# Kernel tuning notes

Measured on AMD Instinct MI355X. Metric: run time of the kernel, lower is better.

## Reference

```python
import jax, jax.numpy as jnp
import numpy as np

N = 200_000      # active voxels
C_IN = 128
C_OUT = 128
GRID = 128
K = 27           # 3x3x3 submanifold kernel offsets
EPS = 1e-4       # scn BatchNormalization default eps
LEAK = 0.333     # scn LeakyReLU default leakiness


def _build_neighbor_idx(rng):
    # unique active voxel coords via unique linear keys in GRID^3
    keys = rng.choice(GRID ** 3, size=N, replace=False).astype(np.int64)
    z = keys % GRID
    y = (keys // GRID) % GRID
    x = keys // (GRID * GRID)
    coords = np.stack([x, y, z], axis=1)  # [N,3]
    order = np.argsort(keys)
    sorted_keys = keys[order]
    offs = np.array([(dx, dy, dz) for dx in (-1, 0, 1)
                     for dy in (-1, 0, 1) for dz in (-1, 0, 1)], dtype=np.int64)
    nb = np.full((N, K), -1, dtype=np.int32)
    for k in range(K):
        q = coords + offs[k]  # [N,3]
        inb = np.all((q >= 0) & (q < GRID), axis=1)
        qk = (q[:, 0] * GRID + q[:, 1]) * GRID + q[:, 2]
        pos = np.searchsorted(sorted_keys, qk)
        pos = np.clip(pos, 0, N - 1)
        hit = inb & (sorted_keys[pos] == qk)
        nb[:, k] = np.where(hit, order[pos].astype(np.int32), -1)
    return nb


def setup_inputs() -> dict:
    key = jax.random.key(0)
    k1, k2 = jax.random.split(key)
    rng = np.random.default_rng(0)
    neighbor_idx = jnp.asarray(_build_neighbor_idx(rng))       # [N,27] int32, -1 = inactive
    features = jax.random.normal(k1, (N, C_IN), dtype=jnp.float32)
    # per-offset conv weights, scn-style init scale
    W = jax.random.normal(k2, (K, C_IN, C_OUT), dtype=jnp.float32) * (1.0 / np.sqrt(K * C_IN))
    b = jnp.zeros((C_OUT,), dtype=jnp.float32)
    gamma = jnp.ones((C_OUT,), dtype=jnp.float32)
    beta = jnp.zeros((C_OUT,), dtype=jnp.float32)
    return {"features": features, "W": W, "b": b, "gamma": gamma,
            "beta": beta, "neighbor_idx": neighbor_idx}


def reference(features, W, b, gamma, beta, neighbor_idx):
    # Submanifold 3D conv: output only at active sites; gather active neighbors.
    valid = (neighbor_idx >= 0)                      # [N,27] bool
    idx = jnp.where(valid, neighbor_idx, 0)          # safe gather index
    out = jnp.broadcast_to(b, (features.shape[0], C_OUT))
    for k in range(K):  # fixed structural loop over 27 kernel offsets
        xk = features[idx[:, k]] * valid[:, k:k + 1].astype(features.dtype)  # [N,C_IN]
        out = out + xk @ W[k]                                                # [N,C_OUT]
    # BatchNormalization over all active sites (training-mode batch stats)
    mean = jnp.mean(out, axis=0)
    var = jnp.var(out, axis=0)
    out = (out - mean) * jax.lax.rsqrt(var + EPS) * gamma + beta
    # LeakyReLU (scn default leakiness 0.333)
    return jnp.where(out > 0, out, LEAK * out)
```

## Files before the change

### kernel.cpp

```cpp
#include <hip/hip_runtime.h>
#include <hip/hip_bf16.h>

#define N_VOX 200000
#define CI 128
#define CO 128
#define KK 27
#define BM 128
#define NBLK 1563
#define NSTEP 54
#define LEAK 0.333f
#define BN_EPS 1e-4f

typedef unsigned short u16;
typedef unsigned int u32;
typedef __attribute__((ext_vector_type(8))) short short8;
typedef __attribute__((ext_vector_type(4))) float f32x4;

typedef const __attribute__((address_space(1))) u32* gptr_t;
typedef __attribute__((address_space(3))) u32* lptr_t;

__device__ __forceinline__ u16 f2bf(float f) {
  union { float f; u32 u; } x; x.f = f;
  return (u16)((x.u + 0x7FFFu + ((x.u >> 16) & 1u)) >> 16);
}
__device__ __forceinline__ u16 cvt_bf(float f) {
  union { __hip_bfloat16 h; u16 u; } c;
  c.h = __float2bfloat16(f);
  return c.u;
}

__global__ __launch_bounds__(256) void fcast_kernel(const float* __restrict__ f,
                                                    u16* __restrict__ fb) {
  size_t i = ((size_t)blockIdx.x * 256 + threadIdx.x) * 8;
  float4 a = *(const float4*)(f + i);
  float4 b = *(const float4*)(f + i + 4);
  u16 t[8];
  t[0] = cvt_bf(a.x); t[1] = cvt_bf(a.y); t[2] = cvt_bf(a.z); t[3] = cvt_bf(a.w);
  t[4] = cvt_bf(b.x); t[5] = cvt_bf(b.y); t[6] = cvt_bf(b.z); t[7] = cvt_bf(b.w);
  *(uint4*)(fb + i) = *(const uint4*)t;
}

__global__ __launch_bounds__(256) void wcast_kernel(const float* __restrict__ W,
                                                    u16* __restrict__ Wt) {
  __shared__ float tile[32][33];
  int k = blockIdx.z;
  int ci0 = blockIdx.y * 32, co0 = blockIdx.x * 32;
  const float* Wk = W + (size_t)k * CI * CO;
  u16* Wtk = Wt + (size_t)k * CI * CO;
  int tx = threadIdx.x, ty = threadIdx.y;
#pragma unroll
  for (int j = 0; j < 4; ++j)
    tile[ty + j * 8][tx] = Wk[(ci0 + ty + j * 8) * CO + co0 + tx];
  __syncthreads();
#pragma unroll
  for (int j = 0; j < 4; ++j) {
    int co = co0 + ty + j * 8;
    int ci = ci0 + tx;
    Wtk[co * CI + (ci ^ ((co & 7) << 3))] = f2bf(tile[tx][ty + j * 8]);
  }
}

__global__ __launch_bounds__(256, 2) void conv_kernel(
    const u16* __restrict__ featb, const u16* __restrict__ Wt,
    const int* __restrict__ nb, const u16* __restrict__ zp,
    float* __restrict__ out, float* __restrict__ partial) {
  __shared__ __align__(16) char smem[79360];
  u16* const Ab0 = (u16*)smem;
  u16* const Ab1 = (u16*)(smem + 16384);
  u16* const Bb0 = (u16*)(smem + 32768);
  u16* const Bb1 = (u16*)(smem + 49152);
  int* const nbs = (int*)(smem + 65536);
  float* const sq = (float*)smem;

  const int tid = threadIdx.x;
  const int bid = blockIdx.x;
  const int row0 = bid * BM;

  for (int i = tid; i < BM * KK; i += 256) {
    int gi = row0 * KK + i;
    nbs[i] = (gi < N_VOX * KK) ? nb[gi] : -1;
  }
  __syncthreads();

  const int lane = tid & 63;
  const int wv = tid >> 6;
  const int wr = wv >> 1, wc = wv & 1;
  const int lr = lane & 15, lg = lane >> 4;

  f32x4 acc[4][4];
#pragma unroll
  for (int m = 0; m < 4; ++m)
#pragma unroll
    for (int n = 0; n < 4; ++n) acc[m][n] = (f32x4){0.f, 0.f, 0.f, 0.f};

  auto issueA = [&](int s, u16* Adst) {
    int k = s >> 1;
    int halfU = (s & 1) * 64;
    int r = tid >> 3;
    int cl = tid & 7;
#pragma unroll
    for (int j = 0; j < 4; ++j) {
      int row = j * 32 + r;
      int src = nbs[row * KK + k];
      const u16* g = (src >= 0) ? (featb + (size_t)src * CI + halfU) : zp;
      g += ((cl ^ (row & 7)) << 3);
      __builtin_amdgcn_global_load_lds((gptr_t)g, (lptr_t)(Adst + (j * 32 + wv * 8) * 64),
                                       16, 0, 0);
    }
  };

  auto issueB = [&](int s, u16* Bdst) {
    int k = s >> 1;
    int halfU = (s & 1) * 64;
    const u16* base = Wt + (size_t)k * CI * CO + halfU;
#pragma unroll
    for (int j = 0; j < 4; ++j) {
      int cb = (j * 4 + wv) * 64;
      int c = cb + lane;
      int co = c >> 3, sub = c & 7;
      __builtin_amdgcn_global_load_lds((gptr_t)(base + co * CI + sub * 8),
                                       (lptr_t)(Bdst + cb * 8), 16, 0, 0);
    }
  };

  auto compute = [&](const u16* A, const u16* B) {
    __builtin_amdgcn_s_setprio(1);
#pragma unroll
    for (int ks = 0; ks < 2; ++ks) {
      short8 a[4], b[4];
#pragma unroll
      for (int m = 0; m < 4; ++m) {
        int r = wr * 64 + m * 16 + lr;
        a[m] = *(const short8*)((const char*)(A + r * 64) +
                                ((ks * 64 + lg * 16) ^ ((r & 7) << 4)));
      }
#pragma unroll
      for (int n = 0; n < 4; ++n) {
        int cn = wc * 64 + n * 16 + lr;
        b[n] = *(const short8*)((const char*)(B + cn * 64) +
                                ((ks * 64 + lg * 16) ^ ((cn & 7) << 4)));
      }
#pragma unroll
      for (int m = 0; m < 4; ++m)
#pragma unroll
        for (int n = 0; n < 4; ++n)
          acc[m][n] = __builtin_amdgcn_mfma_f32_16x16x32_bf16(a[m], b[n], acc[m][n], 0, 0, 0);
    }
    __builtin_amdgcn_s_setprio(0);
  };

  issueA(0, Ab0);
  issueB(0, Bb0);
  for (int s = 0; s < NSTEP; ++s) {
    __syncthreads();
    int pb = s & 1;
    if (s + 1 < NSTEP) {
      issueA(s + 1, pb ? Ab0 : Ab1);
      issueB(s + 1, pb ? Bb0 : Bb1);
    }
    compute(pb ? Ab1 : Ab0, pb ? Bb1 : Bb0);
  }

  float sv[4], qv[4];
#pragma unroll
  for (int n = 0; n < 4; ++n) {
    float s = 0.f, q = 0.f;
    int col = wc * 64 + n * 16 + lr;
#pragma unroll
    for (int m = 0; m < 4; ++m) {
      int rb = row0 + wr * 64 + m * 16 + lg * 4;
#pragma unroll
      for (int e = 0; e < 4; ++e) {
        float x = acc[m][n][e];
        if (rb + e < N_VOX) out[(size_t)(rb + e) * CO + col] = x;
        s += x; q += x * x;
      }
    }
    s += __shfl_xor(s, 16, 64); s += __shfl_xor(s, 32, 64);
    q += __shfl_xor(q, 16, 64); q += __shfl_xor(q, 32, 64);
    sv[n] = s; qv[n] = q;
  }
  __syncthreads();
  if (lg == 0) {
#pragma unroll
    for (int n = 0; n < 4; ++n) {
      int col = wc * 64 + n * 16 + lr;
      sq[wr * 256 + col] = sv[n];
      sq[wr * 256 + 128 + col] = qv[n];
    }
  }
  __syncthreads();
  partial[(size_t)bid * 256 + tid] = sq[tid] + sq[256 + tid];
}

__global__ __launch_bounds__(256, 2) void conv_fb_kernel(
    const float* __restrict__ feat, const u16* __restrict__ Wt,
    const int* __restrict__ nb, float* __restrict__ out,
    float* __restrict__ partial) {
  __shared__ __align__(16) char smem[79360];
  u16* const Ab0 = (u16*)smem;
  u16* const Ab1 = (u16*)(smem + 16384);
  u16* const Bb0 = (u16*)(smem + 32768);
  u16* const Bb1 = (u16*)(smem + 49152);
  int* const nbs = (int*)(smem + 65536);
  float* const sq = (float*)smem;

  const int tid = threadIdx.x;
  const int bid = blockIdx.x;
  const int row0 = bid * BM;

  for (int i = tid; i < BM * KK; i += 256) {
    int gi = row0 * KK + i;
    nbs[i] = (gi < N_VOX * KK) ? nb[gi] : -1;
  }
  __syncthreads();

  const int lane = tid & 63;
  const int wv = tid >> 6;
  const int wr = wv >> 1, wc = wv & 1;
  const int lr = lane & 15, lg = lane >> 4;
  const int arow = tid >> 1;
  const int acol = (tid & 1) * 32;

  f32x4 acc[4][4];
#pragma unroll
  for (int m = 0; m < 4; ++m)
#pragma unroll
    for (int n = 0; n < 4; ++n) acc[m][n] = (f32x4){0.f, 0.f, 0.f, 0.f};

  float4 af[8];
  auto issueA = [&](int s) {
    int k = s >> 1, half = (s & 1) * 64;
    int src = nbs[arow * KK + k];
    if (src >= 0) {
      const float4* p = (const float4*)(feat + (size_t)src * CI + half + acol);
#pragma unroll
      for (int j = 0; j < 8; ++j) af[j] = p[j];
    } else {
#pragma unroll
      for (int j = 0; j < 8; ++j) af[j] = (float4){0.f, 0.f, 0.f, 0.f};
    }
  };
  auto issueB = [&](int s, u16* Bdst) {
    int k = s >> 1, half = (s & 1) * 64;
    const u16* base = Wt + (size_t)k * CO * CI + half;
#pragma unroll
    for (int j = 0; j < 4; ++j) {
      int cb = (j * 4 + wv) * 64;
      int c = cb + lane;
      int co = c >> 3, sub = c & 7;
      __builtin_amdgcn_global_load_lds((gptr_t)(base + co * CI + sub * 8),
                                       (lptr_t)(Bdst + cb * 8), 16, 0, 0);
    }
  };
  auto writeA = [&](u16* Adst) {
    int v = arow & 7;
#pragma unroll
    for (int q = 0; q < 4; ++q) {
      u16 t8[8];
#pragma unroll
      for (int i = 0; i < 2; ++i) {
        float4 f = af[q * 2 + i];
        t8[i * 4 + 0] = cvt_bf(f.x); t8[i * 4 + 1] = cvt_bf(f.y);
        t8[i * 4 + 2] = cvt_bf(f.z); t8[i * 4 + 3] = cvt_bf(f.w);
      }
      int c_o = (tid & 1) * 4 + q;
      *(uint4*)&Adst[arow * 64 + ((c_o ^ v) << 3)] = *(const uint4*)t8;
    }
  };
  auto compute = [&](const u16* A, const u16* B) {
#pragma unroll
    for (int ks = 0; ks < 2; ++ks) {
      short8 a[4], b[4];
#pragma unroll
      for (int m = 0; m < 4; ++m) {
        int r = wr * 64 + m * 16 + lr;
        a[m] = *(const short8*)((const char*)(A + r * 64) +
                                ((ks * 64 + lg * 16) ^ ((r & 7) << 4)));
      }
#pragma unroll
      for (int n = 0; n < 4; ++n) {
        int cn = wc * 64 + n * 16 + lr;
        b[n] = *(const short8*)((const char*)(B + cn * 64) +
                                ((ks * 64 + lg * 16) ^ ((cn & 7) << 4)));
      }
#pragma unroll
      for (int m = 0; m < 4; ++m)
#pragma unroll
        for (int n = 0; n < 4; ++n)
          acc[m][n] = __builtin_amdgcn_mfma_f32_16x16x32_bf16(a[m], b[n], acc[m][n], 0, 0, 0);
    }
  };

  issueA(0);
  issueB(0, Bb0);
  for (int s = 0; s < NSTEP - 1; ++s) {
    int pb = s & 1;
    u16* Ac = pb ? Ab1 : Ab0;
    u16* Bc = pb ? Bb1 : Bb0;
    u16* Bn = pb ? Bb0 : Bb1;
    writeA(Ac);
    __syncthreads();
    issueA(s + 1);
    issueB(s + 1, Bn);
    compute(Ac, Bc);
  }
  writeA(Ab1);
  __syncthreads();
  compute(Ab1, Bb1);

  float sv[4], qv[4];
#pragma unroll
  for (int n = 0; n < 4; ++n) {
    float s = 0.f, q = 0.f;
    int col = wc * 64 + n * 16 + lr;
#pragma unroll
    for (int m = 0; m < 4; ++m) {
      int rb = row0 + wr * 64 + m * 16 + lg * 4;
#pragma unroll
      for (int e = 0; e < 4; ++e) {
        float x = acc[m][n][e];
        if (rb + e < N_VOX) out[(size_t)(rb + e) * CO + col] = x;
        s += x; q += x * x;
      }
    }
    s += __shfl_xor(s, 16, 64); s += __shfl_xor(s, 32, 64);
    q += __shfl_xor(q, 16, 64); q += __shfl_xor(q, 32, 64);
    sv[n] = s; qv[n] = q;
  }
  __syncthreads();
  if (lg == 0) {
#pragma unroll
    for (int n = 0; n < 4; ++n) {
      int col = wc * 64 + n * 16 + lr;
      sq[wr * 256 + col] = sv[n];
      sq[wr * 256 + 128 + col] = qv[n];
    }
  }
  __syncthreads();
  partial[(size_t)bid * 256 + tid] = sq[tid] + sq[256 + tid];
}

__global__ __launch_bounds__(256) void reduce1_kernel(const float* __restrict__ partial,
                                                      float* __restrict__ partial2) {
  int t = threadIdx.x, b = blockIdx.x;
  float acc = 0.f;
  int jend = (b + 1) * 16; if (jend > NBLK) jend = NBLK;
  for (int j = b * 16; j < jend; ++j) acc += partial[(size_t)j * 256 + t];
  partial2[(size_t)b * 256 + t] = acc;
}

__global__ __launch_bounds__(256) void reduce2_kernel(const float* __restrict__ partial2,
                                                      const float* __restrict__ gamma,
                                                      const float* __restrict__ beta,
                                                      float* __restrict__ stats) {
  __shared__ float sums[256];
  int t = threadIdx.x;
  float acc = 0.f;
  for (int j = 0; j < 98; ++j) acc += partial2[(size_t)j * 256 + t];
  sums[t] = acc;
  __syncthreads();
  if (t < 128) {
    float mean = sums[t] / (float)N_VOX;
    float var = sums[128 + t] / (float)N_VOX - mean * mean;
    float scale = gamma[t] * rsqrtf(var + BN_EPS);
    stats[t] = scale;
    stats[128 + t] = beta[t] - mean * scale;
  }
}

__global__ __launch_bounds__(256) void bnact_kernel(float* __restrict__ out,
                                                    const float* __restrict__ stats) {
  __shared__ float s_scale[128], s_shift[128];
  int t = threadIdx.x;
  if (t < 128) { s_scale[t] = stats[t]; s_shift[t] = stats[128 + t]; }
  __syncthreads();
  size_t i = (size_t)blockIdx.x * 256 + t;
  float4* o4 = (float4*)out;
  float4 v = o4[i];
  int c0 = ((int)(i & 31)) << 2;
  float x;
  x = v.x * s_scale[c0 + 0] + s_shift[c0 + 0]; v.x = x > 0.f ? x : LEAK * x;
  x = v.y * s_scale[c0 + 1] + s_shift[c0 + 1]; v.y = x > 0.f ? x : LEAK * x;
  x = v.z * s_scale[c0 + 2] + s_shift[c0 + 2]; v.z = x > 0.f ? x : LEAK * x;
  x = v.w * s_scale[c0 + 3] + s_shift[c0 + 3]; v.w = x > 0.f ? x : LEAK * x;
  o4[i] = v;
}

extern "C" void kernel_launch(void* const* d_in, const int* in_sizes, int n_in,
                              void* d_out, int out_size, void* d_ws, size_t ws_size,
                              hipStream_t stream) {
  const float* feat  = (const float*)d_in[0];
  const float* W     = (const float*)d_in[1];
  const float* gamma = (const float*)d_in[3];
  const float* beta  = (const float*)d_in[4];
  const int*   nb    = (const int*)d_in[5];
  float* out = (float*)d_out;

  char* ws = (char*)d_ws;
  u16*   Wt       = (u16*)ws;
  float* partial  = (float*)(ws + 884736);
  float* partial2 = (float*)(ws + 2485248);
  float* stats    = (float*)(ws + 2585600);
  u16*   zp       = (u16*)(ws + 2586624);
  u16*   featb    = (u16*)(ws + 2586880);
  const size_t need_fast = 2586880u + 51200000u;

  hipLaunchKernelGGL(wcast_kernel, dim3(4, 4, 27), dim3(32, 8), 0, stream, W, Wt);
  if (ws_size >= need_fast) {
    hipMemsetAsync(zp, 0, 256, stream);
    hipLaunchKernelGGL(fcast_kernel, dim3(12500), dim3(256), 0, stream, feat, featb);
    hipLaunchKernelGGL(conv_kernel, dim3(NBLK), dim3(256), 0, stream,
                       featb, Wt, nb, zp, out, partial);
  } else {
    hipLaunchKernelGGL(conv_fb_kernel, dim3(NBLK), dim3(256), 0, stream,
                       feat, Wt, nb, out, partial);
  }
  hipLaunchKernelGGL(reduce1_kernel, dim3(98), dim3(256), 0, stream, partial, partial2);
  hipLaunchKernelGGL(reduce2_kernel, dim3(1), dim3(256), 0, stream, partial2, gamma, beta, stats);
  hipLaunchKernelGGL(bnact_kernel, dim3(25000), dim3(256), 0, stream, out, stats);
}
```

Before: 288.9 us.

## Pre-swizzle weights into MFMA fragment layout and deepen the A-gather pipeline

Weights are now pre-cast into a layout matching the MFMA B-operand fragments. Each wave loads its B fragments straight from global memory into registers, so B no longer goes through LDS. The A gather buffer goes from double to four-deep, staged with global_load_lds and a manual vmcnt wait plus a raw barrier, so three steps of gathers are in flight while MFMAs run. This removes LDS traffic and ds_reads for B and hides gather latency better, at the cost of more VGPRs for two B register sets and redundant B loads per wave from L2.

Result: slower. 303.7 us, median of 2 (+5.1%).

```diff
diff --git a/kernel.cpp b/kernel.cpp
--- a/kernel.cpp
+++ b/kernel.cpp
@@ -40,35 +40,26 @@
   *(uint4*)(fb + i) = *(const uint4*)t;
 }
 
-__global__ __launch_bounds__(256) void wcast_kernel(const float* __restrict__ W,
-                                                    u16* __restrict__ Wt) {
-  __shared__ float tile[32][33];
-  int k = blockIdx.z;
-  int ci0 = blockIdx.y * 32, co0 = blockIdx.x * 32;
+__global__ __launch_bounds__(256) void wcast2_kernel(const float* __restrict__ W,
+                                                     u16* __restrict__ Wt2) {
+  int gid = blockIdx.x * 256 + threadIdx.x;
+  int lane = gid & 63, chunk = gid >> 6;
+  int n8 = chunk & 7, ks = (chunk >> 3) & 1, half = (chunk >> 4) & 1, k = chunk >> 5;
+  int lr = lane & 15, lg = lane >> 4;
+  int co = n8 * 16 + lr;
+  int ci0 = half * 64 + ks * 32 + lg * 8;
   const float* Wk = W + (size_t)k * CI * CO;
-  u16* Wtk = Wt + (size_t)k * CI * CO;
-  int tx = threadIdx.x, ty = threadIdx.y;
-#pragma unroll
-  for (int j = 0; j < 4; ++j)
-    tile[ty + j * 8][tx] = Wk[(ci0 + ty + j * 8) * CO + co0 + tx];
-  __syncthreads();
-#pragma unroll
-  for (int j = 0; j < 4; ++j) {
-    int co = co0 + ty + j * 8;
-    int ci = ci0 + tx;
-    Wtk[co * CI + (ci ^ ((co & 7) << 3))] = f2bf(tile[tx][ty + j * 8]);
-  }
+  u16 t[8];
+#pragma unroll
+  for (int e = 0; e < 8; ++e) t[e] = f2bf(Wk[(ci0 + e) * CO + co]);
+  *(uint4*)(Wt2 + (size_t)gid * 8) = *(const uint4*)t;
 }
 
 __global__ __launch_bounds__(256, 2) void conv_kernel(
-    const u16* __restrict__ featb, const u16* __restrict__ Wt,
+    const u16* __restrict__ featb, const u16* __restrict__ Wt2,
     const int* __restrict__ nb, const u16* __restrict__ zp,
     float* __restrict__ out, float* __restrict__ partial) {
   __shared__ __align__(16) char smem[79360];
-  u16* const Ab0 = (u16*)smem;
-  u16* const Ab1 = (u16*)(smem + 16384);
-  u16* const Bb0 = (u16*)(smem + 32768);
-  u16* const Bb1 = (u16*)(smem + 49152);
   int* const nbs = (int*)(smem + 65536);
   float* const sq = (float*)smem;
 
@@ -93,11 +84,14 @@
 #pragma unroll
     for (int n = 0; n < 4; ++n) acc[m][n] = (f32x4){0.f, 0.f, 0.f, 0.f};
 
-  auto issueA = [&](int s, u16* Adst) {
+  short8 b0[8], b1[8];
+
+  auto issueA = [&](int s, int slot) {
+    if (s >= NSTEP) s = NSTEP - 1;
     int k = s >> 1;
     int halfU = (s & 1) * 64;
-    int r = tid >> 3;
-    int cl = tid & 7;
+    u16* Adst = (u16*)(smem + slot * 16384);
+    int r = tid >> 3, cl = tid & 7;
 #pragma unroll
     for (int j = 0; j < 4; ++j) {
       int row = j * 32 + r;
@@ -109,56 +103,55 @@
     }
   };
 
-  auto issueB = [&](int s, u16* Bdst) {
-    int k = s >> 1;
-    int halfU = (s & 1) * 64;
-    const u16* base = Wt + (size_t)k * CI * CO + halfU;
-#pragma unroll
-    for (int j = 0; j < 4; ++j) {
-      int cb = (j * 4 + wv) * 64;
-      int c = cb + lane;
-      int co = c >> 3, sub = c & 7;
-      __builtin_amdgcn_global_load_lds((gptr_t)(base + co * CI + sub * 8),
-                                       (lptr_t)(Bdst + cb * 8), 16, 0, 0);
-    }
-  };
-
-  auto compute = [&](const u16* A, const u16* B) {
+  auto loadB = [&](int s, short8* bn) {
+    if (s >= NSTEP) s = NSTEP - 1;
+    int k = s >> 1, half = s & 1;
+    const u16* base = Wt2 + (((k * 2 + half) * 16 + wc * 4) * 512) + lane * 8;
+#pragma unroll
+    for (int n = 0; n < 4; ++n)
+#pragma unroll
+      for (int ks = 0; ks < 2; ++ks)
+        bn[n * 2 + ks] = *(const short8*)(base + (ks * 8 + n) * 512);
+  };
+
+  auto compute = [&](int slot, const short8* bc) {
+    const char* A = smem + slot * 16384;
     __builtin_amdgcn_s_setprio(1);
 #pragma unroll
     for (int ks = 0; ks < 2; ++ks) {
-      short8 a[4], b[4];
+      short8 a[4];
 #pragma unroll
       for (int m = 0; m < 4; ++m) {
         int r = wr * 64 + m * 16 + lr;
-        a[m] = *(const short8*)((const char*)(A + r * 64) +
-                                ((ks * 64 + lg * 16) ^ ((r & 7) << 4)));
+        a[m] = *(const short8*)(A + r * 128 + ((ks * 64 + lg * 16) ^ ((r & 7) << 4)));
       }
 #pragma unroll
-      for (int n = 0; n < 4; ++n) {
-        int cn = wc * 64 + n * 16 + lr;
-        b[n] = *(const short8*)((const char*)(B + cn * 64) +
-                                ((ks * 64 + lg * 16) ^ ((cn & 7) << 4)));
-      }
-#pragma unroll
       for (int m = 0; m < 4; ++m)
 #pragma unroll
         for (int n = 0; n < 4; ++n)
-          acc[m][n] = __builtin_amdgcn_mfma_f32_16x16x32_bf16(a[m], b[n], acc[m][n], 0, 0, 0);
+          acc[m][n] = __builtin_amdgcn_mfma_f32_16x16x32_bf16(a[m], bc[n * 2 + ks],
+                                                              acc[m][n], 0, 0, 0);
     }
     __builtin_amdgcn_s_setprio(0);
   };
 
-  issueA(0, Ab0);
-  issueB(0, Bb0);
-  for (int s = 0; s < NSTEP; ++s) {
-    __syncthreads();
-    int pb = s & 1;
-    if (s + 1 < NSTEP) {
-      issueA(s + 1, pb ? Ab0 : Ab1);
-      issueB(s + 1, pb ? Bb0 : Bb1);
-    }
-    compute(pb ? Ab1 : Ab0, pb ? Bb1 : Bb0);
+  auto step_body = [&](int s, const short8* bc, short8* bn) {
+    asm volatile("s_waitcnt vmcnt(16)" ::: "memory");
+    __builtin_amdgcn_sched_barrier(0);
+    __builtin_amdgcn_s_barrier();
+    __builtin_amdgcn_sched_barrier(0);
+    loadB(s + 1, bn);
+    issueA(s + 3, (s + 3) & 3);
+    compute(s & 3, bc);
+  };
+
+  issueA(0, 0);
+  issueA(1, 1);
+  loadB(0, b0);
+  issueA(2, 2);
+  for (int s = 0; s < NSTEP; s += 2) {
+    step_body(s, b0, b1);
+    step_body(s + 1, b1, b0);
   }
 
   float sv[4], qv[4];
@@ -194,15 +187,12 @@
 }
 
 __global__ __launch_bounds__(256, 2) void conv_fb_kernel(
-    const float* __restrict__ feat, const u16* __restrict__ Wt,
+    const float* __restrict__ feat, const u16* __restrict__ Wt2,
     const int* __restrict__ nb, float* __restrict__ out,
     float* __restrict__ partial) {
-  __shared__ __align__(16) char smem[79360];
-  u16* const Ab0 = (u16*)smem;
-  u16* const Ab1 = (u16*)(smem + 16384);
-  u16* const Bb0 = (u16*)(smem + 32768);
-  u16* const Bb1 = (u16*)(smem + 49152);
-  int* const nbs = (int*)(smem + 65536);
+  __shared__ __align__(16) char smem[46592];
+  u16* const Ab = (u16*)smem;
+  int* const nbs = (int*)(smem + 32768);
   float* const sq = (float*)smem;
 
   const int tid = threadIdx.x;
@@ -229,7 +219,9 @@
     for (int n = 0; n < 4; ++n) acc[m][n] = (f32x4){0.f, 0.f, 0.f, 0.f};
 
   float4 af[8];
-  auto issueA = [&](int s) {
+  short8 b0[8], b1[8];
+
+  auto issueAf = [&](int s) {
     int k = s >> 1, half = (s & 1) * 64;
     int src = nbs[arow * KK + k];
     if (src >= 0) {
@@ -241,17 +233,14 @@
       for (int j = 0; j < 8; ++j) af[j] = (float4){0.f, 0.f, 0.f, 0.f};
     }
   };
-  auto issueB = [&](int s, u16* Bdst) {
-    int k = s >> 1, half = (s & 1) * 64;
-    const u16* base = Wt + (size_t)k * CO * CI + half;
-#pragma unroll
-    for (int j = 0; j < 4; ++j) {
-      int cb = (j * 4 + wv) * 64;
-      int c = cb + lane;
-      int co = c >> 3, sub = c & 7;
-      __builtin_amdgcn_global_load_lds((gptr_t)(base + co * CI + sub * 8),
-                                       (lptr_t)(Bdst + cb * 8), 16, 0, 0);
-    }
+  auto loadB = [&](int s, short8* bn) {
+    int k = s >> 1, half = s & 1;
+    const u16* base = Wt2 + (((k * 2 + half) * 16 + wc * 4) * 512) + lane * 8;
+#pragma unroll
+    for (int n = 0; n < 4; ++n)
+#pragma unroll
+      for (int ks = 0; ks < 2; ++ks)
+        bn[n * 2 + ks] = *(const short8*)(base + (ks * 8 + n) * 512);
   };
   auto writeA = [&](u16* Adst) {
     int v = arow & 7;
@@ -268,46 +257,40 @@
       *(uint4*)&Adst[arow * 64 + ((c_o ^ v) << 3)] = *(const uint4*)t8;
     }
   };
-  auto compute = [&](const u16* A, const u16* B) {
+  auto compute = [&](const u16* A, const short8* bc) {
 #pragma unroll
     for (int ks = 0; ks < 2; ++ks) {
-      short8 a[4], b[4];
+      short8 a[4];
 #pragma unroll
       for (int m = 0; m < 4; ++m) {
         int r = wr * 64 + m * 16 + lr;
-        a[m] = *(const short8*)((const char*)(A + r * 64) +
+        a[m] = *(const short8*)((const char*)A + r * 128 +
                                 ((ks * 64 + lg * 16) ^ ((r & 7) << 4)));
       }
 #pragma unroll
-      for (int n = 0; n < 4; ++n) {
-        int cn = wc * 64 + n * 16 + lr;
-        b[n] = *(const short8*)((const char*)(B + cn * 64) +
-                                ((ks * 64 + lg * 16) ^ ((cn & 7) << 4)));
-      }
-#pragma unroll
       for (int m = 0; m < 4; ++m)
 #pragma unroll
         for (int n = 0; n < 4; ++n)
-          acc[m][n] = __builtin_amdgcn_mfma_f32_16x16x32_bf16(a[m], b[n], acc[m][n], 0, 0, 0);
-    }
-  };
-
-  issueA(0);
-  issueB(0, Bb0);
-  for (int s = 0; s < NSTEP - 1; ++s) {
-    int pb = s & 1;
-    u16* Ac = pb ? Ab1 : Ab0;
-    u16* Bc = pb ? Bb1 : Bb0;
-    u16* Bn = pb ? Bb0 : Bb1;
-    writeA(Ac);
-    __syncthreads();
-    issueA(s + 1);
-    issueB(s + 1, Bn);
-    compute(Ac, Bc);
-  }
-  writeA(Ab1);
-  __syncthreads();
-  compute(Ab1, Bb1);
+          acc[m][n] = __builtin_amdgcn_mfma_f32_16x16x32_bf16(a[m], bc[n * 2 + ks],
+                                                              acc[m][n], 0, 0, 0);
+    }
+  };
+
+  issueAf(0);
+  loadB(0, b0);
+  for (int s = 0; s + 2 <= NSTEP - 1; s += 2) {
+    writeA(Ab + (s & 1) * 8192); __syncthreads();
+    issueAf(s + 1); loadB(s + 1, b1);
+    compute(Ab + (s & 1) * 8192, b0);
+    writeA(Ab + ((s + 1) & 1) * 8192); __syncthreads();
+    issueAf(s + 2); loadB(s + 2, b0);
+    compute(Ab + ((s + 1) & 1) * 8192, b1);
+  }
+  writeA(Ab); __syncthreads();
+  issueAf(NSTEP - 1); loadB(NSTEP - 1, b1);
+  compute(Ab, b0);
+  writeA(Ab + 8192); __syncthreads();
+  compute(Ab + 8192, b1);
 
   float sv[4], qv[4];
 #pragma unroll
@@ -398,7 +381,7 @@
   float* out = (float*)d_out;
 
   char* ws = (char*)d_ws;
-  u16*   Wt       = (u16*)ws;
+  u16*   Wt2      = (u16*)ws;
   float* partial  = (float*)(ws + 884736);
   float* partial2 = (float*)(ws + 2485248);
   float* stats    = (float*)(ws + 2585600);
@@ -406,15 +389,15 @@
   u16*   featb    = (u16*)(ws + 2586880);
   const size_t need_fast = 2586880u + 51200000u;
 
-  hipLaunchKernelGGL(wcast_kernel, dim3(4, 4, 27), dim3(32, 8), 0, stream, W, Wt);
+  hipLaunchKernelGGL(wcast2_kernel, dim3(216), dim3(256), 0, stream, W, Wt2);
   if (ws_size >= need_fast) {
     hipMemsetAsync(zp, 0, 256, stream);
     hipLaunchKernelGGL(fcast_kernel, dim3(12500), dim3(256), 0, stream, feat, featb);
     hipLaunchKernelGGL(conv_kernel, dim3(NBLK), dim3(256), 0, stream,
-                       featb, Wt, nb, zp, out, partial);
+                       featb, Wt2, nb, zp, out, partial);
   } else {
     hipLaunchKernelGGL(conv_fb_kernel, dim3(NBLK), dim3(256), 0, stream,
-                       feat, Wt, nb, out, partial);
+                       feat, Wt2, nb, out, partial);
   }
   hipLaunchKernelGGL(reduce1_kernel, dim3(98), dim3(256), 0, stream, partial, partial2);
   hipLaunchKernelGGL(reduce2_kernel, dim3(1), dim3(256), 0, stream, partial2, gamma, beta, stats);
```
